# Performance work log

Measured on AMD Instinct MI355X. Metric: run time of the kernel, lower is better.

## Reference

```python
import jax, jax.numpy as jnp
import numpy as np

N, E, IN_DIM, HID, LAYERS = 300000, 600000, 64, 128, 2
BN_EPS = 1e-5

def setup_inputs() -> dict:
    key = jax.random.key(0)
    ks = jax.random.split(key, 8)
    scale_in = 1.0 / np.sqrt(IN_DIM)
    scale_h = 1.0 / np.sqrt(HID)
    return {
        "node_init": jax.random.normal(ks[0], (N, IN_DIM), dtype=jnp.float32),
        "edge_index": jax.random.randint(ks[1], (2, E), 0, N, dtype=jnp.int64),
        "edge_len": jax.random.uniform(ks[2], (E,), dtype=jnp.float32),
        "W_in": jax.random.normal(ks[3], (IN_DIM, HID), dtype=jnp.float32) * scale_in,
        "b_in": jnp.zeros((HID,), dtype=jnp.float32),
        "att_k": jax.random.normal(ks[4], (HID,), dtype=jnp.float32),
        "Wl": jax.random.normal(ks[5], (LAYERS, HID, HID), dtype=jnp.float32) * scale_h,
        "bl": jnp.zeros((LAYERS, HID), dtype=jnp.float32),
        "gamma": jnp.ones((LAYERS, HID), dtype=jnp.float32),
        "beta": jnp.zeros((LAYERS, HID), dtype=jnp.float32),
    }

def reference(node_init, edge_index, edge_len, W_in, b_in, att_k, Wl, bl, gamma, beta):
    src, dst = edge_index[0], edge_index[1]
    inv_len = 1.0 / (1.0 + edge_len)                     # [E]
    inv_sqrt_h = 1.0 / jnp.sqrt(jnp.asarray(HID, node_init.dtype))
    h = node_init @ W_in + b_in                          # [N,H]
    n = h.shape[0]
    for l in range(LAYERS):
        h_src = h[src]                                   # [E,H] gather
        key = (h_src @ att_k) * inv_sqrt_h               # [E]
        w = jnp.exp(key) * inv_len                       # [E]
        agg = jax.ops.segment_sum(w[:, None] * h_src, dst, num_segments=n)  # [N,H]
        h = h + jax.nn.relu(agg) @ Wl[l] + bl[l]
        mean = jnp.mean(h, axis=0)
        var = jnp.mean((h - mean) ** 2, axis=0)          # biased var (BatchNorm training)
        h = (h - mean) * jax.lax.rsqrt(var + BN_EPS) * gamma[l] + beta[l]
    return h
```

## Files before the change

kernel.cpp:

```cpp
#include <hip/hip_runtime.h>
#include <hip/hip_bf16.h>

#define N_NODES 300000
#define N_EDGES 600000
#define IN_DIMC 64
#define HIDC    128
#define NLAYERS 2
#define BN_EPS  1e-5f
#define INV_SQRT_H 0.08838834764831845f
#define NB_SCAN ((N_NODES + 255) / 256)
#define NTILES  (N_NODES / 16)

typedef __bf16 bf16x8 __attribute__((ext_vector_type(8)));
typedef float floatx4 __attribute__((ext_vector_type(4)));

__device__ int   g_row_ptr[N_NODES + 1];
__device__ int   g_cursor[N_NODES];
__device__ __align__(8) int2 g_edge[N_EDGES];
__device__ __align__(8) int2 g_ew[N_EDGES];
__device__ int   g_bsum[NB_SCAN];
__device__ float g_ekey[N_NODES];
__device__ __align__(16) __hip_bfloat16 g_Win_hi[128 * 64];
__device__ __align__(16) __hip_bfloat16 g_Win_lo[128 * 64];
__device__ __align__(16) __hip_bfloat16 g_Wl_hi[NLAYERS * 128 * 128];
__device__ __align__(16) __hip_bfloat16 g_Wl_lo[NLAYERS * 128 * 128];
__device__ float g_stats[NLAYERS * 2 * HIDC];
__device__ __align__(16) float g_bn_sc[NLAYERS * HIDC];
__device__ __align__(16) float g_bn_sh[NLAYERS * HIDC];

__device__ inline void split2(float x, __hip_bfloat16& hi, __hip_bfloat16& lo) {
    hi = __float2bfloat16(x);
    lo = __float2bfloat16(x - __bfloat162float(hi));
}

__global__ void zero_kernel() {
    int i = blockIdx.x * 256 + threadIdx.x;
    if (i < N_NODES) g_cursor[i] = 0;
    if (i < NLAYERS * 2 * HIDC) g_stats[i] = 0.f;
}

__global__ void prep_w_kernel(const float* __restrict__ W_in,
                              const float* __restrict__ Wl)
{
    int id = blockIdx.x * 256 + threadIdx.x;
    if (id < 128 * 64) {
        int n = id >> 6, k = id & 63;
        split2(W_in[k * 128 + n], g_Win_hi[id], g_Win_lo[id]);
    }
    if (id < NLAYERS * 128 * 128) {
        int l = id >> 14, r = id & 16383;
        int n = r >> 7, k = r & 127;
        split2(Wl[l * 16384 + k * 128 + n], g_Wl_hi[id], g_Wl_lo[id]);
    }
}

__global__ void hist_kernel(const int* __restrict__ dst)
{
    int e = blockIdx.x * 256 + threadIdx.x;
    if (e < N_EDGES) atomicAdd(&g_cursor[dst[e]], 1);
}

__global__ void scan1_kernel()
{
    __shared__ int tmp[256];
    int t = threadIdx.x;
    int i = blockIdx.x * 256 + t;
    tmp[t] = (i < N_NODES) ? g_cursor[i] : 0;
    __syncthreads();
    for (int d = 128; d > 0; d >>= 1) {
        if (t < d) tmp[t] += tmp[t + d];
        __syncthreads();
    }
    if (t == 0) g_bsum[blockIdx.x] = tmp[0];
}

__global__ void scan2_kernel()
{
    __shared__ int tmp[256];
    __shared__ int carry;
    int t = threadIdx.x;
    if (t == 0) { carry = 0; g_row_ptr[N_NODES] = N_EDGES; }
    __syncthreads();
    for (int base = 0; base < NB_SCAN; base += 256) {
        int i = base + t;
        int v = (i < NB_SCAN) ? g_bsum[i] : 0;
        tmp[t] = v;
        __syncthreads();
        for (int d = 1; d < 256; d <<= 1) {
            int x = (t >= d) ? tmp[t - d] : 0;
            __syncthreads();
            tmp[t] += x;
            __syncthreads();
        }
        int c = carry;
        if (i < NB_SCAN) g_bsum[i] = c + tmp[t] - v;
        __syncthreads();
        if (t == 0) carry = c + tmp[255];
        __syncthreads();
    }
}

__global__ void scan3_kernel()
{
    __shared__ int tmp[256];
    int t = threadIdx.x;
    int i = blockIdx.x * 256 + t;
    int v = (i < N_NODES) ? g_cursor[i] : 0;
    tmp[t] = v;
    __syncthreads();
    for (int d = 1; d < 256; d <<= 1) {
        int x = (t >= d) ? tmp[t - d] : 0;
        __syncthreads();
        tmp[t] += x;
        __syncthreads();
    }
    int r = g_bsum[blockIdx.x] + tmp[t] - v;
    if (i < N_NODES) { g_row_ptr[i] = r; g_cursor[i] = r; }
}

__global__ void scatter_kernel(const int* __restrict__ src, const int* __restrict__ dst,
                               const float* __restrict__ elen)
{
    int e = blockIdx.x * 256 + threadIdx.x;
    if (e >= N_EDGES) return;
    int d = dst[e];
    int pos = atomicAdd(&g_cursor[d], 1);
    int2 ed;
    ed.x = src[e];
    ed.y = __float_as_int(1.0f / (1.0f + elen[e]));
    g_edge[pos] = ed;
}

__global__ __launch_bounds__(256) void wt_kernel()
{
    int e = blockIdx.x * 256 + threadIdx.x;
    if (e >= N_EDGES) return;
    int2 ed = g_edge[e];
    int2 ew;
    ew.x = ed.x;
    ew.y = __float_as_int(g_ekey[ed.x] * __int_as_float(ed.y));
    g_ew[e] = ew;
}

__global__ __launch_bounds__(256) void edge_csr_kernel(
    const float* __restrict__ h, float* __restrict__ agg, int prev)
{
    int lane = threadIdx.x & 63;
    int n = blockIdx.x * 4 + (threadIdx.x >> 6);
    if (n >= N_NODES) return;
    int beg = g_row_ptr[n], end = g_row_ptr[n + 1];
    float a0 = 0.f, a1 = 0.f, sw = 0.f;
    const float2* h2 = (const float2*)h;
    for (int j = beg; j < end; j += 4) {
        int2 e0 = g_ew[j];
        int2 e1 = (j + 1 < end) ? g_ew[j + 1] : make_int2(e0.x, 0);
        int2 e2 = (j + 2 < end) ? g_ew[j + 2] : make_int2(e0.x, 0);
        int2 e3 = (j + 3 < end) ? g_ew[j + 3] : make_int2(e0.x, 0);
        float w0 = __int_as_float(e0.y);
        float w1 = __int_as_float(e1.y);
        float w2 = __int_as_float(e2.y);
        float w3 = __int_as_float(e3.y);
        float2 x0 = h2[(size_t)e0.x * 64 + lane];
        float2 x1 = h2[(size_t)e1.x * 64 + lane];
        float2 x2 = h2[(size_t)e2.x * 64 + lane];
        float2 x3 = h2[(size_t)e3.x * 64 + lane];
        a0 += w0 * x0.x + w1 * x1.x + w2 * x2.x + w3 * x3.x;
        a1 += w0 * x0.y + w1 * x1.y + w2 * x2.y + w3 * x3.y;
        sw += w0 + w1 + w2 + w3;
    }
    float2 sc = make_float2(1.f, 1.f), sh = make_float2(0.f, 0.f);
    if (prev >= 0) {
        sc = ((const float2*)(g_bn_sc + prev * HIDC))[lane];
        sh = ((const float2*)(g_bn_sh + prev * HIDC))[lane];
    }
    float2 o;
    o.x = fmaxf(sc.x * a0 + sh.x * sw, 0.f);
    o.y = fmaxf(sc.y * a1 + sh.y * sw, 0.f);
    ((float2*)(agg + (size_t)n * HIDC))[lane] = o;
}

__global__ __launch_bounds__(256) void proj_mfma_kernel(
    const float* __restrict__ X, const float* __restrict__ b,
    const float* __restrict__ att_k, float* __restrict__ h)
{
    __shared__ __align__(16) __hip_bfloat16 Ah[64 * 72];
    __shared__ __align__(16) __hip_bfloat16 Al[64 * 72];
    __shared__ __align__(16) __hip_bfloat16 Bh[128 * 72];
    __shared__ __align__(16) __hip_bfloat16 Bl[128 * 72];
    int t = threadIdx.x;
    int nbase = blockIdx.x * 64;

    for (int i = t; i < 1024; i += 256) {
        int row = i >> 3, c8 = i & 7;
        *(float4*)((char*)Bh + row * 144 + c8 * 16) =
            *(const float4*)((const char*)g_Win_hi + row * 128 + c8 * 16);
        *(float4*)((char*)Bl + row * 144 + c8 * 16) =
            *(const float4*)((const char*)g_Win_lo + row * 128 + c8 * 16);
    }
    for (int i = t; i < 1024; i += 256) {
        int row = i >> 4, c4 = i & 15;
        int n = nbase + row;
        float4 v = make_float4(0.f, 0.f, 0.f, 0.f);
        if (n < N_NODES) v = *(const float4*)(X + (size_t)n * IN_DIMC + c4 * 4);
        union { __hip_bfloat16 e[4]; uint2 u; } ph, pl;
        split2(v.x, ph.e[0], pl.e[0]); split2(v.y, ph.e[1], pl.e[1]);
        split2(v.z, ph.e[2], pl.e[2]); split2(v.w, ph.e[3], pl.e[3]);
        *(uint2*)((char*)Ah + row * 144 + c4 * 8) = ph.u;
        *(uint2*)((char*)Al + row * 144 + c4 * 8) = pl.u;
    }
    __syncthreads();

    int lane = t & 63, w = t >> 6;
    int m16 = lane & 15, quad = lane >> 4;
    floatx4 acc[8];
#pragma unroll
    for (int i = 0; i < 8; ++i) acc[i] = floatx4{0.f, 0.f, 0.f, 0.f};

#pragma unroll
    for (int kk = 0; kk < 64; kk += 32) {
        bf16x8 ah = *(const bf16x8*)((const char*)Ah + (w * 16 + m16) * 144 + (kk + quad * 8) * 2);
        bf16x8 al = *(const bf16x8*)((const char*)Al + (w * 16 + m16) * 144 + (kk + quad * 8) * 2);
#pragma unroll
        for (int nt = 0; nt < 8; ++nt) {
            bf16x8 bh = *(const bf16x8*)((const char*)Bh + (nt * 16 + m16) * 144 + (kk + quad * 8) * 2);
            bf16x8 bl = *(const bf16x8*)((const char*)Bl + (nt * 16 + m16) * 144 + (kk + quad * 8) * 2);
            acc[nt] = __builtin_amdgcn_mfma_f32_16x16x32_bf16(ah, bh, acc[nt], 0, 0, 0);
            acc[nt] = __builtin_amdgcn_mfma_f32_16x16x32_bf16(al, bh, acc[nt], 0, 0, 0);
            acc[nt] = __builtin_amdgcn_mfma_f32_16x16x32_bf16(ah, bl, acc[nt], 0, 0, 0);
        }
    }
    float dotr[4] = {0.f, 0.f, 0.f, 0.f};
#pragma unroll
    for (int nt = 0; nt < 8; ++nt) {
        int ch = nt * 16 + m16;
        float bias = b[ch];
        float ak = att_k[ch];
#pragma unroll
        for (int r = 0; r < 4; ++r) {
            int n = nbase + w * 16 + quad * 4 + r;
            float o = acc[nt][r] + bias;
            if (n < N_NODES) h[(size_t)n * HIDC + ch] = o;
            dotr[r] += ak * o;
        }
    }
#pragma unroll
    for (int r = 0; r < 4; ++r) {
        float p = dotr[r];
        p += __shfl_xor(p, 1); p += __shfl_xor(p, 2);
        p += __shfl_xor(p, 4); p += __shfl_xor(p, 8);
        int n = nbase + w * 16 + quad * 4 + r;
        if (m16 == 0 && n < N_NODES) g_ekey[n] = __expf(p * INV_SQRT_H);
    }
}

__global__ __launch_bounds__(256) void key_kernel(const float* __restrict__ h,
                                                  const float* __restrict__ att_k,
                                                  int prev)
{
    int t = threadIdx.x;
    int lane = t & 63;
    int half = lane >> 5, sub = lane & 31;
    int n = (blockIdx.x * 4 + (t >> 6)) * 2 + half;
    if (n >= N_NODES) return;
    float4 x = ((const float4*)h)[(size_t)n * 32 + sub];
    float4 sc = ((const float4*)(g_bn_sc + prev * HIDC))[sub];
    float4 sh = ((const float4*)(g_bn_sh + prev * HIDC))[sub];
    float4 ak = ((const float4*)att_k)[sub];
    float p = (sc.x * x.x + sh.x) * ak.x + (sc.y * x.y + sh.y) * ak.y +
              (sc.z * x.z + sh.z) * ak.z + (sc.w * x.w + sh.w) * ak.w;
    p += __shfl_xor(p, 1);  p += __shfl_xor(p, 2);
    p += __shfl_xor(p, 4);  p += __shfl_xor(p, 8);
    p += __shfl_xor(p, 16);
    if (sub == 0) g_ekey[n] = __expf(p * INV_SQRT_H);
}

__global__ __launch_bounds__(256) void layer_gemm_kernel(
    float* __restrict__ h, const float* __restrict__ agg,
    const float* __restrict__ b, int layer, int prev)
{
    __shared__ __align__(16) __hip_bfloat16 Bh[128 * 136];
    __shared__ __align__(16) __hip_bfloat16 Bl[128 * 136];
    __shared__ float red[256];
    int t = threadIdx.x;
    const __hip_bfloat16* Wh = g_Wl_hi + layer * 16384;
    const __hip_bfloat16* Wlo = g_Wl_lo + layer * 16384;
    red[t] = 0.f;

    for (int i = t; i < 2048; i += 256) {
        int row = i >> 4, c8 = i & 15;
        *(float4*)((char*)Bh + row * 272 + c8 * 16) =
            *(const float4*)((const char*)Wh + row * 256 + c8 * 16);
        *(float4*)((char*)Bl + row * 272 + c8 * 16) =
            *(const float4*)((const char*)Wlo + row * 256 + c8 * 16);
    }
    __syncthreads();

    const int lane = t & 63, w = t >> 6;
    const int m16 = lane & 15, quad = lane >> 4;
    const int wid = blockIdx.x * 4 + w;
    const int nwaves = gridDim.x * 4;

    float bias[8], scp[8], shp[8];
#pragma unroll
    for (int nt = 0; nt < 8; ++nt) {
        int ch = nt * 16 + m16;
        bias[nt] = b[ch];
        scp[nt] = (prev >= 0) ? g_bn_sc[prev * HIDC + ch] : 1.f;
        shp[nt] = (prev >= 0) ? g_bn_sh[prev * HIDC + ch] : 0.f;
    }
    float sreg[8], qreg[8];
#pragma unroll
    for (int nt = 0; nt < 8; ++nt) { sreg[nt] = 0.f; qreg[nt] = 0.f; }

    for (int tile = wid; tile < NTILES; tile += nwaves) {
        const float* arow = agg + (size_t)(tile * 16 + m16) * HIDC + quad * 8;
        floatx4 acc[8];
#pragma unroll
        for (int i = 0; i < 8; ++i) acc[i] = floatx4{0.f, 0.f, 0.f, 0.f};

#pragma unroll
        for (int kk = 0; kk < 4; ++kk) {
            float4 a0 = *(const float4*)(arow + kk * 32);
            float4 a1 = *(const float4*)(arow + kk * 32 + 4);
            union { __hip_bfloat16 e[8]; bf16x8 v; } ah, al;
            split2(a0.x, ah.e[0], al.e[0]); split2(a0.y, ah.e[1], al.e[1]);
            split2(a0.z, ah.e[2], al.e[2]); split2(a0.w, ah.e[3], al.e[3]);
            split2(a1.x, ah.e[4], al.e[4]); split2(a1.y, ah.e[5], al.e[5]);
            split2(a1.z, ah.e[6], al.e[6]); split2(a1.w, ah.e[7], al.e[7]);
#pragma unroll
            for (int nt = 0; nt < 8; ++nt) {
                bf16x8 bh = *(const bf16x8*)((const char*)Bh + (nt * 16 + m16) * 272 + (kk * 32 + quad * 8) * 2);
                bf16x8 bl = *(const bf16x8*)((const char*)Bl + (nt * 16 + m16) * 272 + (kk * 32 + quad * 8) * 2);
                acc[nt] = __builtin_amdgcn_mfma_f32_16x16x32_bf16(ah.v, bh, acc[nt], 0, 0, 0);
                acc[nt] = __builtin_amdgcn_mfma_f32_16x16x32_bf16(al.v, bh, acc[nt], 0, 0, 0);
                acc[nt] = __builtin_amdgcn_mfma_f32_16x16x32_bf16(ah.v, bl, acc[nt], 0, 0, 0);
            }
        }
        int node0 = tile * 16 + quad * 4;
#pragma unroll
        for (int nt = 0; nt < 8; ++nt) {
            int ch = nt * 16 + m16;
#pragma unroll
            for (int r = 0; r < 4; ++r) {
                float* hp = h + (size_t)(node0 + r) * HIDC + ch;
                float o = scp[nt] * (*hp) + shp[nt] + acc[nt][r] + bias[nt];
                *hp = o;
                sreg[nt] += o;
                qreg[nt] += o * o;
            }
        }
    }

#pragma unroll
    for (int nt = 0; nt < 8; ++nt) {
        float s = sreg[nt], q = qreg[nt];
        s += __shfl_xor(s, 16); s += __shfl_xor(s, 32);
        q += __shfl_xor(q, 16); q += __shfl_xor(q, 32);
        if (quad == 0) {
            atomicAdd(&red[nt * 16 + m16], s);
            atomicAdd(&red[HIDC + nt * 16 + m16], q);
        }
    }
    __syncthreads();
    atomicAdd(&g_stats[layer * 2 * HIDC + t], red[t]);
}

__global__ void bn_prep_kernel(const float* __restrict__ gamma,
                               const float* __restrict__ beta, int layer)
{
    int c = threadIdx.x;
    if (c >= HIDC) return;
    const float invN = 1.0f / (float)N_NODES;
    float mean = g_stats[layer * 2 * HIDC + c] * invN;
    float var = g_stats[layer * 2 * HIDC + HIDC + c] * invN - mean * mean;
    float s = gamma[layer * HIDC + c] * rsqrtf(var + BN_EPS);
    g_bn_sc[layer * HIDC + c] = s;
    g_bn_sh[layer * HIDC + c] = beta[layer * HIDC + c] - mean * s;
}

__global__ __launch_bounds__(256) void bn_apply_kernel(float* __restrict__ h, int layer)
{
    size_t idx = (size_t)blockIdx.x * 256 + threadIdx.x;
    if (idx >= (size_t)N_NODES * (HIDC / 4)) return;
    int cg = (int)(idx & 31);
    float4 sc = ((const float4*)(g_bn_sc + layer * HIDC))[cg];
    float4 sh = ((const float4*)(g_bn_sh + layer * HIDC))[cg];
    float4 v = ((float4*)h)[idx];
    v.x = sc.x * v.x + sh.x;
    v.y = sc.y * v.y + sh.y;
    v.z = sc.z * v.z + sh.z;
    v.w = sc.w * v.w + sh.w;
    ((float4*)h)[idx] = v;
}

extern "C" void kernel_launch(void* const* d_in, const int* in_sizes, int n_in,
                              void* d_out, int out_size, void* d_ws, size_t ws_size,
                              hipStream_t stream) {
    (void)in_sizes; (void)n_in; (void)out_size; (void)ws_size;
    const float* node_init = (const float*)d_in[0];
    const int*   eidx      = (const int*)d_in[1];
    const float* elen      = (const float*)d_in[2];
    const float* W_in      = (const float*)d_in[3];
    const float* b_in      = (const float*)d_in[4];
    const float* att_k     = (const float*)d_in[5];
    const float* Wl        = (const float*)d_in[6];
    const float* bl        = (const float*)d_in[7];
    const float* gamma     = (const float*)d_in[8];
    const float* beta      = (const float*)d_in[9];

    float* h   = (float*)d_out;
    float* agg = (float*)d_ws;

    const int* src = eidx;
    const int* dst = eidx + N_EDGES;

    zero_kernel<<<NB_SCAN, 256, 0, stream>>>();
    hist_kernel<<<(N_EDGES + 255) / 256, 256, 0, stream>>>(dst);
    scan1_kernel<<<NB_SCAN, 256, 0, stream>>>();
    scan2_kernel<<<1, 256, 0, stream>>>();
    scan3_kernel<<<NB_SCAN, 256, 0, stream>>>();
    scatter_kernel<<<(N_EDGES + 255) / 256, 256, 0, stream>>>(src, dst, elen);
    prep_w_kernel<<<(NLAYERS * 128 * 128 + 255) / 256, 256, 0, stream>>>(W_in, Wl);

    proj_mfma_kernel<<<(N_NODES + 63) / 64, 256, 0, stream>>>(node_init, b_in, att_k, h);

    for (int l = 0; l < NLAYERS; ++l) {
        if (l > 0)
            key_kernel<<<(N_NODES / 2 + 3) / 4, 256, 0, stream>>>(h, att_k, l - 1);
        wt_kernel<<<(N_EDGES + 255) / 256, 256, 0, stream>>>();
        edge_csr_kernel<<<(N_NODES + 3) / 4, 256, 0, stream>>>(h, agg, l - 1);
        layer_gemm_kernel<<<512, 256, 0, stream>>>(h, agg, bl + (size_t)l * HIDC, l, l - 1);
        bn_prep_kernel<<<1, 128, 0, stream>>>(gamma, beta, l);
    }
    bn_apply_kernel<<<(N_NODES * (HIDC / 4) + 255) / 256, 256, 0, stream>>>(h, NLAYERS - 1);
}
```

Baseline: 927.5 us.

## Split agg into bf16 hi/lo in edge kernel; register-resident weights in layer GEMM

The edge aggregation kernel now writes agg as two bf16 arrays (hi and lo) instead of fp32, so the hi/lo split is done once at the producer rather than in the GEMM. The layer GEMM drops the shared-memory weight copy. Each wave holds its 32-channel slice of the hi/lo weights in registers, and a block of 4 waves covers all 128 output channels of a 16-node tile. BN statistics now go straight to global atomics instead of a shared reduction, the grid grows to 768 blocks, and launch bounds are set for 3 blocks per SM. This costs more register pressure and more global atomics.

```diff
diff --git a/kernel.cpp b/kernel.cpp
--- a/kernel.cpp
+++ b/kernel.cpp
@@ -143,7 +143,8 @@
 }
 
 __global__ __launch_bounds__(256) void edge_csr_kernel(
-    const float* __restrict__ h, float* __restrict__ agg, int prev)
+    const float* __restrict__ h, __hip_bfloat16* __restrict__ agg_hi,
+    __hip_bfloat16* __restrict__ agg_lo, int prev)
 {
     int lane = threadIdx.x & 63;
     int n = blockIdx.x * 4 + (threadIdx.x >> 6);
@@ -173,10 +174,13 @@
         sc = ((const float2*)(g_bn_sc + prev * HIDC))[lane];
         sh = ((const float2*)(g_bn_sh + prev * HIDC))[lane];
     }
-    float2 o;
-    o.x = fmaxf(sc.x * a0 + sh.x * sw, 0.f);
-    o.y = fmaxf(sc.y * a1 + sh.y * sw, 0.f);
-    ((float2*)(agg + (size_t)n * HIDC))[lane] = o;
+    float o0 = fmaxf(sc.x * a0 + sh.x * sw, 0.f);
+    float o1 = fmaxf(sc.y * a1 + sh.y * sw, 0.f);
+    union { __hip_bfloat16 e[2]; unsigned u; } ph, pl;
+    split2(o0, ph.e[0], pl.e[0]);
+    split2(o1, ph.e[1], pl.e[1]);
+    ((unsigned*)agg_hi)[(size_t)n * 64 + lane] = ph.u;
+    ((unsigned*)agg_lo)[(size_t)n * 64 + lane] = pl.u;
 }
 
 __global__ __launch_bounds__(256) void proj_mfma_kernel(
@@ -274,72 +278,54 @@
     if (sub == 0) g_ekey[n] = __expf(p * INV_SQRT_H);
 }
 
-__global__ __launch_bounds__(256) void layer_gemm_kernel(
-    float* __restrict__ h, const float* __restrict__ agg,
+__global__ __launch_bounds__(256, 3) void layer_gemm_kernel(
+    float* __restrict__ h, const __hip_bfloat16* __restrict__ agg_hi,
+    const __hip_bfloat16* __restrict__ agg_lo,
     const float* __restrict__ b, int layer, int prev)
 {
-    __shared__ __align__(16) __hip_bfloat16 Bh[128 * 136];
-    __shared__ __align__(16) __hip_bfloat16 Bl[128 * 136];
-    __shared__ float red[256];
-    int t = threadIdx.x;
-    const __hip_bfloat16* Wh = g_Wl_hi + layer * 16384;
-    const __hip_bfloat16* Wlo = g_Wl_lo + layer * 16384;
-    red[t] = 0.f;
-
-    for (int i = t; i < 2048; i += 256) {
-        int row = i >> 4, c8 = i & 15;
-        *(float4*)((char*)Bh + row * 272 + c8 * 16) =
-            *(const float4*)((const char*)Wh + row * 256 + c8 * 16);
-        *(float4*)((char*)Bl + row * 272 + c8 * 16) =
-            *(const float4*)((const char*)Wlo + row * 256 + c8 * 16);
-    }
-    __syncthreads();
-
+    const int t = threadIdx.x;
     const int lane = t & 63, w = t >> 6;
     const int m16 = lane & 15, quad = lane >> 4;
-    const int wid = blockIdx.x * 4 + w;
-    const int nwaves = gridDim.x * 4;
-
-    float bias[8], scp[8], shp[8];
-#pragma unroll
-    for (int nt = 0; nt < 8; ++nt) {
-        int ch = nt * 16 + m16;
+
+    bf16x8 bh[2][4], blv[2][4];
+    float bias[2], scp[2], shp[2];
+#pragma unroll
+    for (int nt = 0; nt < 2; ++nt) {
+        int ch = w * 32 + nt * 16 + m16;
+        const __hip_bfloat16* Wh  = g_Wl_hi + layer * 16384 + ch * 128 + quad * 8;
+        const __hip_bfloat16* Wl2 = g_Wl_lo + layer * 16384 + ch * 128 + quad * 8;
+#pragma unroll
+        for (int kk = 0; kk < 4; ++kk) {
+            bh[nt][kk]  = *(const bf16x8*)(Wh  + kk * 32);
+            blv[nt][kk] = *(const bf16x8*)(Wl2 + kk * 32);
+        }
         bias[nt] = b[ch];
         scp[nt] = (prev >= 0) ? g_bn_sc[prev * HIDC + ch] : 1.f;
         shp[nt] = (prev >= 0) ? g_bn_sh[prev * HIDC + ch] : 0.f;
     }
-    float sreg[8], qreg[8];
-#pragma unroll
-    for (int nt = 0; nt < 8; ++nt) { sreg[nt] = 0.f; qreg[nt] = 0.f; }
-
-    for (int tile = wid; tile < NTILES; tile += nwaves) {
-        const float* arow = agg + (size_t)(tile * 16 + m16) * HIDC + quad * 8;
-        floatx4 acc[8];
-#pragma unroll
-        for (int i = 0; i < 8; ++i) acc[i] = floatx4{0.f, 0.f, 0.f, 0.f};
-
+    float sreg[2] = {0.f, 0.f}, qreg[2] = {0.f, 0.f};
+
+    for (int tile = blockIdx.x; tile < NTILES; tile += gridDim.x) {
+        const __hip_bfloat16* ahp = agg_hi + (size_t)(tile * 16 + m16) * HIDC + quad * 8;
+        const __hip_bfloat16* alp = agg_lo + (size_t)(tile * 16 + m16) * HIDC + quad * 8;
+        floatx4 acc[2];
+        acc[0] = floatx4{0.f, 0.f, 0.f, 0.f};
+        acc[1] = floatx4{0.f, 0.f, 0.f, 0.f};
 #pragma unroll
         for (int kk = 0; kk < 4; ++kk) {
-            float4 a0 = *(const float4*)(arow + kk * 32);
-            float4 a1 = *(const float4*)(arow + kk * 32 + 4);
-            union { __hip_bfloat16 e[8]; bf16x8 v; } ah, al;
-            split2(a0.x, ah.e[0], al.e[0]); split2(a0.y, ah.e[1], al.e[1]);
-            split2(a0.z, ah.e[2], al.e[2]); split2(a0.w, ah.e[3], al.e[3]);
-            split2(a1.x, ah.e[4], al.e[4]); split2(a1.y, ah.e[5], al.e[5]);
-            split2(a1.z, ah.e[6], al.e[6]); split2(a1.w, ah.e[7], al.e[7]);
-#pragma unroll
-            for (int nt = 0; nt < 8; ++nt) {
-                bf16x8 bh = *(const bf16x8*)((const char*)Bh + (nt * 16 + m16) * 272 + (kk * 32 + quad * 8) * 2);
-                bf16x8 bl = *(const bf16x8*)((const char*)Bl + (nt * 16 + m16) * 272 + (kk * 32 + quad * 8) * 2);
-                acc[nt] = __builtin_amdgcn_mfma_f32_16x16x32_bf16(ah.v, bh, acc[nt], 0, 0, 0);
-                acc[nt] = __builtin_amdgcn_mfma_f32_16x16x32_bf16(al.v, bh, acc[nt], 0, 0, 0);
-                acc[nt] = __builtin_amdgcn_mfma_f32_16x16x32_bf16(ah.v, bl, acc[nt], 0, 0, 0);
+            bf16x8 ah = *(const bf16x8*)(ahp + kk * 32);
+            bf16x8 al = *(const bf16x8*)(alp + kk * 32);
+#pragma unroll
+            for (int nt = 0; nt < 2; ++nt) {
+                acc[nt] = __builtin_amdgcn_mfma_f32_16x16x32_bf16(ah, bh[nt][kk],  acc[nt], 0, 0, 0);
+                acc[nt] = __builtin_amdgcn_mfma_f32_16x16x32_bf16(al, bh[nt][kk],  acc[nt], 0, 0, 0);
+                acc[nt] = __builtin_amdgcn_mfma_f32_16x16x32_bf16(ah, blv[nt][kk], acc[nt], 0, 0, 0);
             }
         }
         int node0 = tile * 16 + quad * 4;
 #pragma unroll
-        for (int nt = 0; nt < 8; ++nt) {
-            int ch = nt * 16 + m16;
+        for (int nt = 0; nt < 2; ++nt) {
+            int ch = w * 32 + nt * 16 + m16;
 #pragma unroll
             for (int r = 0; r < 4; ++r) {
                 float* hp = h + (size_t)(node0 + r) * HIDC + ch;
@@ -352,17 +338,16 @@
     }
 
 #pragma unroll
-    for (int nt = 0; nt < 8; ++nt) {
+    for (int nt = 0; nt < 2; ++nt) {
         float s = sreg[nt], q = qreg[nt];
         s += __shfl_xor(s, 16); s += __shfl_xor(s, 32);
         q += __shfl_xor(q, 16); q += __shfl_xor(q, 32);
         if (quad == 0) {
-            atomicAdd(&red[nt * 16 + m16], s);
-            atomicAdd(&red[HIDC + nt * 16 + m16], q);
-        }
-    }
-    __syncthreads();
-    atomicAdd(&g_stats[layer * 2 * HIDC + t], red[t]);
+            int ch = w * 32 + nt * 16 + m16;
+            atomicAdd(&g_stats[layer * 2 * HIDC + ch], s);
+            atomicAdd(&g_stats[layer * 2 * HIDC + HIDC + ch], q);
+        }
+    }
 }
 
 __global__ void bn_prep_kernel(const float* __restrict__ gamma,
@@ -408,8 +393,9 @@
     const float* gamma     = (const float*)d_in[8];
     const float* beta      = (const float*)d_in[9];
 
-    float* h   = (float*)d_out;
-    float* agg = (float*)d_ws;
+    float* h = (float*)d_out;
+    __hip_bfloat16* agg_hi = (__hip_bfloat16*)d_ws;
+    __hip_bfloat16* agg_lo = agg_hi + (size_t)N_NODES * HIDC;
 
     const int* src = eidx;
     const int* dst = eidx + N_EDGES;
@@ -428,8 +414,8 @@
         if (l > 0)
             key_kernel<<<(N_NODES / 2 + 3) / 4, 256, 0, stream>>>(h, att_k, l - 1);
         wt_kernel<<<(N_EDGES + 255) / 256, 256, 0, stream>>>();
-        edge_csr_kernel<<<(N_NODES + 3) / 4, 256, 0, stream>>>(h, agg, l - 1);
-        layer_gemm_kernel<<<512, 256, 0, stream>>>(h, agg, bl + (size_t)l * HIDC, l, l - 1);
+        edge_csr_kernel<<<(N_NODES + 3) / 4, 256, 0, stream>>>(h, agg_hi, agg_lo, l - 1);
+        layer_gemm_kernel<<<768, 256, 0, stream>>>(h, agg_hi, agg_lo, bl + (size_t)l * HIDC, l, l - 1);
         bn_prep_kernel<<<1, 128, 0, stream>>>(gamma, beta, l);
     }
     bn_apply_kernel<<<(N_NODES * (HIDC / 4) + 255) / 256, 256, 0, stream>>>(h, NLAYERS - 1);
```

Result: slower. 949.7 us (+2.4%).
